# Kernel optimization log

Hardware: AMD Instinct MI355X
Metric: run time of the kernel (lower is better)

Reference implementation:

```python
import jax, jax.numpy as jnp
import numpy as np

BATCH = 1048576
IN_DIM = 28
BOND = 10
OUT = 10

def setup_inputs() -> dict:
    key = jax.random.key(0)
    k1, k2, k3 = jax.random.split(key, 3)
    inputs = jax.random.uniform(k1, (BATCH, 2 * IN_DIM), dtype=jnp.float32)
    t0 = jax.random.uniform(k2, (IN_DIM, BOND), dtype=jnp.float32)
    t1 = jax.random.uniform(k3, (IN_DIM, BOND, OUT), dtype=jnp.float32)
    bias = jnp.zeros((OUT,), dtype=jnp.float32)
    return {"inputs": inputs, "t0": t0, "t1": t1, "bias": bias}

def reference(inputs, t0, t1, bias):
    # Reshape each sample to (units=2, in_dim); contract each physical leg,
    # then contract the shared bond between the two MPO tensors.
    x = inputs.reshape(-1, 2, IN_DIM)          # [n, 2, i]
    h0 = jnp.einsum('ni,ib->nb', x[:, 0], t0)   # [n, bond]
    h1 = jnp.einsum('nj,jbo->nbo', x[:, 1], t1) # [n, bond, out]
    c = jnp.einsum('nb,nbo->no', h0, h1) + bias # [n, out]
    return jax.nn.sigmoid(c)
```

## Files before the change

kernel.cpp:

```cpp
#include <hip/hip_runtime.h>
#include <math.h>

#define IN_DIM 28
#define BOND   10
#define OUT_D  10
#define BLOCK  256
#define H0_STRIDE 11

__global__ __launch_bounds__(BLOCK) void tn_kernel(
    const float* __restrict__ x,
    const float* __restrict__ t0,
    const float* __restrict__ t1,
    const float* __restrict__ bias,
    float* __restrict__ out,
    int n_total)
{
    __shared__ __align__(16) float lt0[IN_DIM * BOND];
    __shared__ __align__(16) float lt1[BOND * IN_DIM * OUT_D];
    __shared__ float lbias[OUT_D];
    __shared__ float lh0[BLOCK * H0_STRIDE];

    const int tid = threadIdx.x;

    for (int idx = tid; idx < IN_DIM * BOND; idx += BLOCK)
        lt0[idx] = t0[idx];
    for (int idx = tid; idx < BOND * IN_DIM * OUT_D; idx += BLOCK) {
        const int b = idx / (IN_DIM * OUT_D);
        const int r = idx - b * (IN_DIM * OUT_D);
        const int j = r / OUT_D;
        const int o = r - j * OUT_D;
        lt1[idx] = t1[(j * BOND + b) * OUT_D + o];
    }
    if (tid < OUT_D) lbias[tid] = bias[tid];

    const int n = blockIdx.x * BLOCK + tid;

    float4 xq[14];
    const float4* __restrict__ xrow =
        reinterpret_cast<const float4*>(x + (size_t)n * (2 * IN_DIM));
#pragma unroll
    for (int k = 0; k < 14; ++k) xq[k] = xrow[k];

    __syncthreads();

    float xe[2 * IN_DIM];
#pragma unroll
    for (int k = 0; k < 14; ++k) {
        xe[4 * k + 0] = xq[k].x;
        xe[4 * k + 1] = xq[k].y;
        xe[4 * k + 2] = xq[k].z;
        xe[4 * k + 3] = xq[k].w;
    }

    float h0[BOND];
#pragma unroll
    for (int b = 0; b < BOND; ++b) h0[b] = 0.0f;
    {
        const float4* __restrict__ w0 = reinterpret_cast<const float4*>(lt0);
#pragma unroll
        for (int c = 0; c < 70; ++c) {
            const float4 w = w0[c];
            const int f = 4 * c;
            h0[(f + 0) % 10] = fmaf(xe[(f + 0) / 10], w.x, h0[(f + 0) % 10]);
            h0[(f + 1) % 10] = fmaf(xe[(f + 1) / 10], w.y, h0[(f + 1) % 10]);
            h0[(f + 2) % 10] = fmaf(xe[(f + 2) / 10], w.z, h0[(f + 2) % 10]);
            h0[(f + 3) % 10] = fmaf(xe[(f + 3) / 10], w.w, h0[(f + 3) % 10]);
        }
    }
#pragma unroll
    for (int b = 0; b < BOND; ++b) lh0[tid * H0_STRIDE + b] = h0[b];

    float acc[OUT_D];
#pragma unroll
    for (int o = 0; o < OUT_D; ++o) acc[o] = lbias[o];

#pragma unroll 1
    for (int b = 0; b < BOND; ++b) {
        const float hb = lh0[tid * H0_STRIDE + b];
        const float4* __restrict__ wb =
            reinterpret_cast<const float4*>(&lt1[b * (IN_DIM * OUT_D)]);
        float h1[OUT_D];
#pragma unroll
        for (int o = 0; o < OUT_D; ++o) h1[o] = 0.0f;
#pragma unroll
        for (int c = 0; c < 70; ++c) {
            const float4 w = wb[c];
            const int f = 4 * c;
            h1[(f + 0) % 10] = fmaf(xe[28 + (f + 0) / 10], w.x, h1[(f + 0) % 10]);
            h1[(f + 1) % 10] = fmaf(xe[28 + (f + 1) / 10], w.y, h1[(f + 1) % 10]);
            h1[(f + 2) % 10] = fmaf(xe[28 + (f + 2) / 10], w.z, h1[(f + 2) % 10]);
            h1[(f + 3) % 10] = fmaf(xe[28 + (f + 3) / 10], w.w, h1[(f + 3) % 10]);
        }
#pragma unroll
        for (int o = 0; o < OUT_D; ++o) acc[o] = fmaf(hb, h1[o], acc[o]);
    }

    if (n < n_total) {
        float2* __restrict__ op =
            reinterpret_cast<float2*>(out + (size_t)n * OUT_D);
#pragma unroll
        for (int o = 0; o < OUT_D; o += 2) {
            float2 r;
            r.x = 1.0f / (1.0f + __expf(-acc[o]));
            r.y = 1.0f / (1.0f + __expf(-acc[o + 1]));
            op[o >> 1] = r;
        }
    }
}

extern "C" void kernel_launch(void* const* d_in, const int* in_sizes, int n_in,
                              void* d_out, int out_size, void* d_ws, size_t ws_size,
                              hipStream_t stream) {
    const float* x    = (const float*)d_in[0];
    const float* t0   = (const float*)d_in[1];
    const float* t1   = (const float*)d_in[2];
    const float* bias = (const float*)d_in[3];
    float* out        = (float*)d_out;

    const int n_total = in_sizes[0] / (2 * IN_DIM);
    const int grid = (n_total + BLOCK - 1) / BLOCK;
    tn_kernel<<<grid, BLOCK, 0, stream>>>(x, t0, t1, bias, out, n_total);
}
```

Measured before the change: 353.3 us.

## Read weights directly from global memory instead of staging in LDS

Drops the shared-memory staging of t0, t1 and bias, along with the block barrier and the LDS spill of h0. Weights are now read straight from global memory with wave-uniform addresses, so they can become scalar loads served from cache. h0 is computed per bond inside the loop rather than up front. This removes the per-block LDS fill and shared-memory traffic, but the per-element weight loads become scalar/global loads that may add latency and reduce vector-width loading.

```diff
diff --git a/kernel.cpp b/kernel.cpp
--- a/kernel.cpp
+++ b/kernel.cpp
@@ -5,7 +5,6 @@
 #define BOND   10
 #define OUT_D  10
 #define BLOCK  256
-#define H0_STRIDE 11
 
 __global__ __launch_bounds__(BLOCK) void tn_kernel(
     const float* __restrict__ x,
@@ -15,24 +14,7 @@
     float* __restrict__ out,
     int n_total)
 {
-    __shared__ __align__(16) float lt0[IN_DIM * BOND];
-    __shared__ __align__(16) float lt1[BOND * IN_DIM * OUT_D];
-    __shared__ float lbias[OUT_D];
-    __shared__ float lh0[BLOCK * H0_STRIDE];
-
     const int tid = threadIdx.x;
-
-    for (int idx = tid; idx < IN_DIM * BOND; idx += BLOCK)
-        lt0[idx] = t0[idx];
-    for (int idx = tid; idx < BOND * IN_DIM * OUT_D; idx += BLOCK) {
-        const int b = idx / (IN_DIM * OUT_D);
-        const int r = idx - b * (IN_DIM * OUT_D);
-        const int j = r / OUT_D;
-        const int o = r - j * OUT_D;
-        lt1[idx] = t1[(j * BOND + b) * OUT_D + o];
-    }
-    if (tid < OUT_D) lbias[tid] = bias[tid];
-
     const int n = blockIdx.x * BLOCK + tid;
 
     float4 xq[14];
@@ -40,8 +22,6 @@
         reinterpret_cast<const float4*>(x + (size_t)n * (2 * IN_DIM));
 #pragma unroll
     for (int k = 0; k < 14; ++k) xq[k] = xrow[k];
-
-    __syncthreads();
 
     float xe[2 * IN_DIM];
 #pragma unroll
@@ -52,45 +32,30 @@
         xe[4 * k + 3] = xq[k].w;
     }
 
-    float h0[BOND];
-#pragma unroll
-    for (int b = 0; b < BOND; ++b) h0[b] = 0.0f;
-    {
-        const float4* __restrict__ w0 = reinterpret_cast<const float4*>(lt0);
-#pragma unroll
-        for (int c = 0; c < 70; ++c) {
-            const float4 w = w0[c];
-            const int f = 4 * c;
-            h0[(f + 0) % 10] = fmaf(xe[(f + 0) / 10], w.x, h0[(f + 0) % 10]);
-            h0[(f + 1) % 10] = fmaf(xe[(f + 1) / 10], w.y, h0[(f + 1) % 10]);
-            h0[(f + 2) % 10] = fmaf(xe[(f + 2) / 10], w.z, h0[(f + 2) % 10]);
-            h0[(f + 3) % 10] = fmaf(xe[(f + 3) / 10], w.w, h0[(f + 3) % 10]);
-        }
-    }
-#pragma unroll
-    for (int b = 0; b < BOND; ++b) lh0[tid * H0_STRIDE + b] = h0[b];
-
     float acc[OUT_D];
 #pragma unroll
-    for (int o = 0; o < OUT_D; ++o) acc[o] = lbias[o];
+    for (int o = 0; o < OUT_D; ++o) acc[o] = bias[o];
 
 #pragma unroll 1
     for (int b = 0; b < BOND; ++b) {
-        const float hb = lh0[tid * H0_STRIDE + b];
-        const float4* __restrict__ wb =
-            reinterpret_cast<const float4*>(&lt1[b * (IN_DIM * OUT_D)]);
+        const float* __restrict__ w0b = t0 + b;
+        float hb = 0.0f;
+#pragma unroll
+        for (int i = 0; i < IN_DIM; ++i)
+            hb = fmaf(xe[i], w0b[i * BOND], hb);
+
+        const float* __restrict__ wb = t1 + b * OUT_D;
         float h1[OUT_D];
 #pragma unroll
         for (int o = 0; o < OUT_D; ++o) h1[o] = 0.0f;
 #pragma unroll
-        for (int c = 0; c < 70; ++c) {
-            const float4 w = wb[c];
-            const int f = 4 * c;
-            h1[(f + 0) % 10] = fmaf(xe[28 + (f + 0) / 10], w.x, h1[(f + 0) % 10]);
-            h1[(f + 1) % 10] = fmaf(xe[28 + (f + 1) / 10], w.y, h1[(f + 1) % 10]);
-            h1[(f + 2) % 10] = fmaf(xe[28 + (f + 2) / 10], w.z, h1[(f + 2) % 10]);
-            h1[(f + 3) % 10] = fmaf(xe[28 + (f + 3) / 10], w.w, h1[(f + 3) % 10]);
+        for (int j = 0; j < IN_DIM; ++j) {
+            const float x1j = xe[IN_DIM + j];
+#pragma unroll
+            for (int o = 0; o < OUT_D; ++o)
+                h1[o] = fmaf(x1j, wb[j * (BOND * OUT_D) + o], h1[o]);
         }
+
 #pragma unroll
         for (int o = 0; o < OUT_D; ++o) acc[o] = fmaf(hb, h1[o], acc[o]);
     }
```

Measured after the change: 361.1 us. 2.2% more time.
